# Kernel optimization log

Measured on AMD Instinct MI355X. Metric: run time of the kernel, lower is better.

The kernel has to match this reference:

```python
import jax, jax.numpy as jnp
import numpy as np

B, T, C = 4, 2048, 768
H = 12
D = C // H  # head dim 64

def setup_inputs() -> dict:
    key = jax.random.key(0)
    ks = jax.random.split(key, 6)
    scale = 1.0 / np.sqrt(C)
    x = jax.random.normal(ks[0], (B, T, C), dtype=jnp.float32)
    attention_mask = jax.random.randint(ks[1], (B, T), 0, 2, dtype=jnp.int64)
    Wqkv = jax.random.normal(ks[2], (C, 3 * C), dtype=jnp.float32) * scale
    bqkv = jax.random.normal(ks[3], (3 * C,), dtype=jnp.float32) * 0.02
    Wo = jax.random.normal(ks[4], (C, C), dtype=jnp.float32) * scale
    bo = jax.random.normal(ks[5], (C,), dtype=jnp.float32) * 0.02
    return {"x": x, "attention_mask": attention_mask, "Wqkv": Wqkv,
            "bqkv": bqkv, "Wo": Wo, "bo": bo}

def reference(x, attention_mask, Wqkv, bqkv, Wo, bo):
    # fused QKV projection: [B,T,3C]
    qkv = jnp.einsum('btc,cd->btd', x, Wqkv) + bqkv
    q, k, v = jnp.split(qkv, 3, axis=-1)
    # reshape to [B,H,T,D]
    q = q.reshape(B, T, H, D).transpose(0, 2, 1, 3)
    k = k.reshape(B, T, H, D).transpose(0, 2, 1, 3)
    v = v.reshape(B, T, H, D).transpose(0, 2, 1, 3)
    # module quirk: True (attended) where attention_mask == 0
    keep = (attention_mask == 0)[:, None, None, :]  # [B,1,1,T]
    scores = jnp.einsum('bhqd,bhkd->bhqk', q, k) / np.sqrt(D)
    scores = jnp.where(keep, scores, jnp.finfo(scores.dtype).min)
    probs = jax.nn.softmax(scores, axis=-1)
    context = jnp.einsum('bhqk,bhkd->bhqd', probs, v)
    context = context.transpose(0, 2, 1, 3).reshape(B, T, C)
    return jnp.einsum('btc,cd->btd', context, Wo) + bo
```

## Files before the change

kernel.cpp:

```cpp
#include <hip/hip_runtime.h>
#include <stdint.h>

#define AS1 __attribute__((address_space(1)))
#define AS3 __attribute__((address_space(3)))

typedef _Float16 f16;
typedef _Float16 f16x8 __attribute__((ext_vector_type(8)));
typedef _Float16 f16x4 __attribute__((ext_vector_type(4)));
typedef _Float16 f16x2 __attribute__((ext_vector_type(2)));
typedef float    f32x4  __attribute__((ext_vector_type(4)));
typedef float    f32x16 __attribute__((ext_vector_type(16)));

#define B_  4
#define T_  2048
#define C_  768
#define H_  12
#define D_  64
#define M_  (B_*T_)
#define N1_ (3*C_)

__device__ __forceinline__ void g2l16(const void* g, void* l) {
  __builtin_amdgcn_global_load_lds((const AS1 void*)g, (AS3 void*)l, 16, 0, 0);
}

__device__ __forceinline__ f32x4 fzero4() { f32x4 z = {0.f, 0.f, 0.f, 0.f}; return z; }

__device__ __forceinline__ f16x2 pk_f16(float a, float b) {
  auto t = __builtin_amdgcn_cvt_pkrtz(a, b);
  return *(f16x2*)&t;
}

__global__ __launch_bounds__(256)
void transpose_cvt_k(const float* __restrict__ in, f16* __restrict__ out, int R, int C) {
  __shared__ float tile[32][33];
  const int tx = threadIdx.x & 31, ty = threadIdx.x >> 5;
  const int c0 = blockIdx.x * 32, r0 = blockIdx.y * 32;
#pragma unroll
  for (int i = 0; i < 32; i += 8)
    tile[ty + i][tx] = in[(long)(r0 + ty + i) * C + c0 + tx];
  __syncthreads();
#pragma unroll
  for (int i = 0; i < 32; i += 8)
    out[(long)(c0 + ty + i) * R + r0 + tx] = (f16)tile[tx][ty + i];
}

__global__ __launch_bounds__(256)
void convert_f32_f16(const float* __restrict__ in, f16* __restrict__ out) {
  const int i = (blockIdx.x * 256 + threadIdx.x) * 4;
  const float4 v = *(const float4*)(in + i);
  f16x4 o = {(f16)v.x, (f16)v.y, (f16)v.z, (f16)v.w};
  *(f16x4*)(out + i) = o;
}

__global__ __launch_bounds__(256)
void init_idx_kernel(int* __restrict__ idx, int* __restrict__ cnt) {
  const int g = blockIdx.x * 256 + threadIdx.x;
  idx[g] = 0;
  if (g < B_) cnt[g] = 0;
}

__global__ __launch_bounds__(256)
void compact_kernel(const int* __restrict__ mask, int* __restrict__ idx,
                    int* __restrict__ cnt) {
  const int b = blockIdx.y;
  const int t = blockIdx.x * 256 + threadIdx.x;
  if (mask[b * T_ + t] == 0) {
    const int s = atomicAdd(&cnt[b], 1);
    idx[b * T_ + s] = t;
  }
}

__global__ __launch_bounds__(256)
void build_vt_gather(const f16* __restrict__ qkv, const int* __restrict__ idx,
                     const int* __restrict__ cnt, f16* __restrict__ vt) {
  __shared__ f16 tile[32][33];
  const int z = blockIdx.z, b = z / H_, h = z % H_;
  const int s0 = blockIdx.x * 32, d0 = blockIdx.y * 32;
  if (s0 >= cnt[b]) return;
  const int tx = threadIdx.x & 31, ty = threadIdx.x >> 5;
  const int* idx_b = idx + b * T_;
  f16* dst = vt + (long)z * D_ * T_;
#pragma unroll
  for (int i = 0; i < 32; i += 8) {
    const int t = idx_b[s0 + ty + i];
    tile[ty + i][tx] = qkv[(long)(b * T_ + t) * N1_ + 2 * C_ + h * D_ + d0 + tx];
  }
  __syncthreads();
#pragma unroll
  for (int i = 0; i < 32; i += 8)
    dst[(long)(d0 + ty + i) * T_ + s0 + tx] = tile[tx][ty + i];
}

template <typename OutT>
__global__ __launch_bounds__(256)
void gemm_bias_kernel(const f16* __restrict__ A, const f16* __restrict__ Bt,
                      const float* __restrict__ bias, OutT* __restrict__ Cc,
                      int K, int ldc) {
  __shared__ f16 lA[128 * 32];
  __shared__ f16 lB[128 * 32];
  const int tid = threadIdx.x;
  const int n0 = blockIdx.x * 128, m0 = blockIdx.y * 128;
  const int lane = tid & 63, w = tid >> 6;
  const int wm = (w & 1) * 64, wn = (w >> 1) * 64;
  const int r15 = lane & 15, q4 = lane >> 4;

  const int c0 = tid, c1 = 256 + tid;
  const int ar0 = c0 >> 2, ak0 = (c0 & 3) * 8;
  const int ar1 = c1 >> 2, ak1 = (c1 & 3) * 8;
  const f16* Ab = A + (long)m0 * K;
  const f16* Bb = Bt + (long)n0 * K;

  f32x4 acc[4][4];
#pragma unroll
  for (int i = 0; i < 4; i++)
#pragma unroll
    for (int j = 0; j < 4; j++) acc[i][j] = fzero4();

  for (int kb = 0; kb < K; kb += 32) {
    g2l16(Ab + (long)ar0 * K + kb + ak0, &lA[c0 * 8]);
    g2l16(Ab + (long)ar1 * K + kb + ak1, &lA[c1 * 8]);
    g2l16(Bb + (long)ar0 * K + kb + ak0, &lB[c0 * 8]);
    g2l16(Bb + (long)ar1 * K + kb + ak1, &lB[c1 * 8]);
    __syncthreads();
    f16x8 af[4], bfv[4];
#pragma unroll
    for (int mi = 0; mi < 4; mi++)
      af[mi] = *(const f16x8*)&lA[(wm + mi * 16 + r15) * 32 + q4 * 8];
#pragma unroll
    for (int ni = 0; ni < 4; ni++)
      bfv[ni] = *(const f16x8*)&lB[(wn + ni * 16 + r15) * 32 + q4 * 8];
#pragma unroll
    for (int mi = 0; mi < 4; mi++)
#pragma unroll
      for (int ni = 0; ni < 4; ni++)
        acc[mi][ni] = __builtin_amdgcn_mfma_f32_16x16x32_f16(af[mi], bfv[ni], acc[mi][ni], 0, 0, 0);
    __syncthreads();
  }

#pragma unroll
  for (int ni = 0; ni < 4; ni++) {
    const int col = n0 + wn + ni * 16 + r15;
    const float bs = bias[col];
#pragma unroll
    for (int mi = 0; mi < 4; mi++) {
#pragma unroll
      for (int r = 0; r < 4; r++) {
        const int row = m0 + wm + mi * 16 + q4 * 4 + r;
        Cc[(long)row * ldc + col] = (OutT)(acc[mi][ni][r] + bs);
      }
    }
  }
}

__global__ __launch_bounds__(256, 4)
void attn_kernel(const f16* __restrict__ qkv, const f16* __restrict__ vtc,
                 const int* __restrict__ idx, const int* __restrict__ cnt,
                 f16* __restrict__ ctx) {
  const int LDS_ = 72;
  __shared__ f16 QPs[128 * 72];
  __shared__ f16 Ks[64 * 72], Vs[64 * 72];
  const int tid = threadIdx.x, lane = tid & 63, w = tid >> 6;
  const int l31 = lane & 31, hh = lane >> 5;
  const int bh = blockIdx.y, b = bh / H_, h = bh % H_;
  const int q0 = blockIdx.x * 128;
  const f16* Qg = qkv + (long)(b * T_ + q0) * N1_ + h * D_;
  const f16* Kbase = qkv + (long)b * T_ * N1_ + C_ + h * D_;
  const f16* Vg = vtc + (long)bh * D_ * T_;
  const int* idx_b = idx + b * T_;
  const int nk = cnt[b];
  const int nkt = (nk + 63) >> 6;

  const f16 qsc = (f16)0.18033688f;
#pragma unroll
  for (int i = 0; i < 4; i++) {
    int c = i * 256 + tid, r = c >> 3, dcq = (c & 7) * 8;
    f16x8 v = *(const f16x8*)(Qg + (long)r * N1_ + dcq);
#pragma unroll
    for (int j = 0; j < 8; j++) v[j] = v[j] * qsc;
    *(f16x8*)&QPs[r * LDS_ + dcq] = v;
  }
  __syncthreads();
  f16x8 bq[4];
#pragma unroll
  for (int j = 0; j < 4; j++)
    bq[j] = *(const f16x8*)&QPs[(w * 32 + l31) * LDS_ + j * 16 + hh * 8];

  const int r0 = tid >> 3, r1 = 32 + (tid >> 3), dc = (tid & 7) * 8;
  int idxp0 = idx_b[r0], idxp1 = idx_b[r1];

  float l_acc = 0.f;
  f32x16 O[2];
#pragma unroll
  for (int dt = 0; dt < 2; dt++)
#pragma unroll
    for (int r = 0; r < 16; r++) O[dt][r] = 0.f;

  for (int kt = 0; kt < (nkt << 6); kt += 64) {
    __syncthreads();
    {
      const int t0 = idxp0, t1 = idxp1;
      f16x8 kv0 = *(const f16x8*)(Kbase + (long)t0 * N1_ + dc);
      f16x8 kv1 = *(const f16x8*)(Kbase + (long)t1 * N1_ + dc);
      f16x8 vv0 = *(const f16x8*)(Vg + (long)r0 * T_ + kt + dc);
      f16x8 vv1 = *(const f16x8*)(Vg + (long)r1 * T_ + kt + dc);
      idxp0 = idx_b[min(kt + 64 + r0, T_ - 1)];
      idxp1 = idx_b[min(kt + 64 + r1, T_ - 1)];
      *(f16x8*)&Ks[r0 * LDS_ + dc] = kv0;
      *(f16x8*)&Ks[r1 * LDS_ + dc] = kv1;
      *(f16x8*)&Vs[r0 * LDS_ + dc] = vv0;
      *(f16x8*)&Vs[r1 * LDS_ + dc] = vv1;
    }
    __syncthreads();

    const bool full = (kt + 64 <= nk);
#pragma unroll
    for (int ktile = 0; ktile < 2; ktile++) {
      f32x16 acc;
      if (full) {
#pragma unroll
        for (int r = 0; r < 16; r++) acc[r] = 0.f;
      } else {
        const int kbase = kt + ktile * 32 + hh * 4;
#pragma unroll
        for (int g = 0; g < 4; g++)
#pragma unroll
          for (int i = 0; i < 4; i++)
            acc[4 * g + i] = (kbase + 8 * g + i < nk) ? 0.f : -1e30f;
      }
#pragma unroll
      for (int j = 0; j < 4; j++) {
        f16x8 ak = *(const f16x8*)&Ks[(ktile * 32 + l31) * LDS_ + j * 16 + hh * 8];
        acc = __builtin_amdgcn_mfma_f32_32x32x16_f16(ak, bq[j], acc, 0, 0, 0);
      }
#pragma unroll
      for (int g = 0; g < 4; g++) {
        const float p0 = __builtin_amdgcn_exp2f(acc[4 * g + 0]);
        const float p1 = __builtin_amdgcn_exp2f(acc[4 * g + 1]);
        const float p2 = __builtin_amdgcn_exp2f(acc[4 * g + 2]);
        const float p3 = __builtin_amdgcn_exp2f(acc[4 * g + 3]);
        l_acc += (p0 + p1) + (p2 + p3);
        const f16x2 lo = pk_f16(p0, p1), hi = pk_f16(p2, p3);
        f16x4 pv; pv[0] = lo[0]; pv[1] = lo[1]; pv[2] = hi[0]; pv[3] = hi[1];
        *(f16x4*)&QPs[(w * 32 + l31) * LDS_ + ktile * 32 + g * 8 + hh * 4] = pv;
      }
    }
    asm volatile("s_waitcnt lgkmcnt(0)" ::: "memory");

#pragma unroll
    for (int j = 0; j < 4; j++) {
      f16x8 pa = *(const f16x8*)&QPs[(w * 32 + l31) * LDS_ + j * 16 + hh * 8];
#pragma unroll
      for (int dt = 0; dt < 2; dt++) {
        f16x8 vb = *(const f16x8*)&Vs[(dt * 32 + l31) * LDS_ + j * 16 + hh * 8];
        O[dt] = __builtin_amdgcn_mfma_f32_32x32x16_f16(pa, vb, O[dt], 0, 0, 0);
      }
    }
  }

  l_acc += __shfl_xor(l_acc, 32);
  float* Lw = (float*)&QPs[(w * 32) * LDS_];
  asm volatile("s_waitcnt lgkmcnt(0)" ::: "memory");
  if (hh == 0) Lw[l31] = l_acc;
  asm volatile("s_waitcnt lgkmcnt(0)" ::: "memory");
#pragma unroll
  for (int g = 0; g < 4; g++) {
    const f32x4 lv = *(const f32x4*)&Lw[g * 8 + hh * 4];
#pragma unroll
    for (int i = 0; i < 4; i++) {
      const float inv = 1.f / lv[i];
      const int row = b * T_ + q0 + w * 32 + g * 8 + hh * 4 + i;
#pragma unroll
      for (int dt = 0; dt < 2; dt++)
        ctx[(long)row * C_ + h * D_ + dt * 32 + l31] = (f16)(O[dt][4 * g + i] * inv);
    }
  }
}

extern "C" void kernel_launch(void* const* d_in, const int* in_sizes, int n_in,
                              void* d_out, int out_size, void* d_ws, size_t ws_size,
                              hipStream_t stream) {
  (void)in_sizes; (void)n_in; (void)out_size; (void)ws_size;
  const float* x    = (const float*)d_in[0];
  const int*   mask = (const int*)  d_in[1];
  const float* Wqkv = (const float*)d_in[2];
  const float* bqkv = (const float*)d_in[3];
  const float* Wo   = (const float*)d_in[4];
  const float* bo   = (const float*)d_in[5];
  float* out = (float*)d_out;

  char* ws = (char*)d_ws;
  const size_t OFF_WQKVT = 0;
  const size_t OFF_WOT   = OFF_WQKVT + 3538944;
  const size_t OFF_QKV   = OFF_WOT + 1179648;
  const size_t OFF_VT    = OFF_QKV + 37748736;
  const size_t OFF_XH    = OFF_VT + 12582912;
  const size_t OFF_IDX   = OFF_XH + 12582912;
  const size_t OFF_CNT   = OFF_IDX + 32768;
  f16* WqkvT = (f16*)(ws + OFF_WQKVT);
  f16* WoT   = (f16*)(ws + OFF_WOT);
  f16* qkv   = (f16*)(ws + OFF_QKV);
  f16* Vtc   = (f16*)(ws + OFF_VT);
  f16* xh    = (f16*)(ws + OFF_XH);
  f16* ctx   = (f16*)(ws + OFF_XH);
  int* idx   = (int*)(ws + OFF_IDX);
  int* cnt   = (int*)(ws + OFF_CNT);

  transpose_cvt_k<<<dim3(72, 24), 256, 0, stream>>>(Wqkv, WqkvT, 768, 2304);
  transpose_cvt_k<<<dim3(24, 24), 256, 0, stream>>>(Wo, WoT, 768, 768);
  convert_f32_f16<<<dim3(M_ * C_ / 1024), 256, 0, stream>>>(x, xh);
  init_idx_kernel<<<dim3(B_ * T_ / 256), 256, 0, stream>>>(idx, cnt);
  compact_kernel<<<dim3(T_ / 256, B_), 256, 0, stream>>>(mask, idx, cnt);
  gemm_bias_kernel<f16><<<dim3(18, 64), 256, 0, stream>>>(xh, WqkvT, bqkv, qkv, 768, 2304);
  build_vt_gather<<<dim3(64, 2, 48), 256, 0, stream>>>(qkv, idx, cnt, Vtc);
  attn_kernel<<<dim3(16, 48), 256, 0, stream>>>(qkv, Vtc, idx, cnt, ctx);
  gemm_bias_kernel<float><<<dim3(6, 64), 256, 0, stream>>>(ctx, WoT, bo, out, 768, 768);
}
```

Before: 215.0 us.

## Compute K/V projection only for kept tokens and store compacted K/V

The QKV GEMM is split so Q is computed for all rows, while K and V are computed only for unmasked tokens, using the compacted index list as a row gather on A. K and V are then written in compacted, contiguous form, so the attention kernel no longer does indexed gathers for K and build_vt reads V sequentially. This skips roughly half of the K/V projection work and makes K loads in attention contiguous. It relies on padding tiles (rows past cnt) being consistent, since the tail of the last tile reads padded idx entries that are set to zero.

```diff
diff --git a/kernel.cpp b/kernel.cpp
--- a/kernel.cpp
+++ b/kernel.cpp
@@ -71,20 +71,17 @@
 }
 
 __global__ __launch_bounds__(256)
-void build_vt_gather(const f16* __restrict__ qkv, const int* __restrict__ idx,
-                     const int* __restrict__ cnt, f16* __restrict__ vt) {
+void build_vt(const f16* __restrict__ Vc, const int* __restrict__ cnt,
+              f16* __restrict__ vt) {
   __shared__ f16 tile[32][33];
   const int z = blockIdx.z, b = z / H_, h = z % H_;
   const int s0 = blockIdx.x * 32, d0 = blockIdx.y * 32;
-  if (s0 >= cnt[b]) return;
+  if (s0 >= ((cnt[b] + 63) & ~63)) return;
   const int tx = threadIdx.x & 31, ty = threadIdx.x >> 5;
-  const int* idx_b = idx + b * T_;
   f16* dst = vt + (long)z * D_ * T_;
 #pragma unroll
-  for (int i = 0; i < 32; i += 8) {
-    const int t = idx_b[s0 + ty + i];
-    tile[ty + i][tx] = qkv[(long)(b * T_ + t) * N1_ + 2 * C_ + h * D_ + d0 + tx];
-  }
+  for (int i = 0; i < 32; i += 8)
+    tile[ty + i][tx] = Vc[(long)(b * T_ + s0 + ty + i) * C_ + h * D_ + d0 + tx];
   __syncthreads();
 #pragma unroll
   for (int i = 0; i < 32; i += 8)
@@ -152,9 +149,95 @@
   }
 }
 
+__global__ __launch_bounds__(256)
+void gemm_qkv_kernel(const f16* __restrict__ A, const f16* __restrict__ Bt,
+                     const float* __restrict__ bias, f16* __restrict__ Qb,
+                     f16* __restrict__ Kc, f16* __restrict__ Vc,
+                     const int* __restrict__ idx, const int* __restrict__ cnt) {
+  const int K = C_;
+  __shared__ f16 lA[128 * 32];
+  __shared__ f16 lB[128 * 32];
+  const int tid = threadIdx.x;
+  const bool isQ = blockIdx.x < 6;
+  const int n0 = (isQ ? blockIdx.x : blockIdx.x - 6) * 128;
+  const int lane = tid & 63, w = tid >> 6;
+  const int wm = (w & 1) * 64, wn = (w >> 1) * 64;
+  const int r15 = lane & 15, q4 = lane >> 4;
+
+  const int c0 = tid, c1 = 256 + tid;
+  const int ar0 = c0 >> 2, ak0 = (c0 & 3) * 8;
+  const int ar1 = c1 >> 2, ak1 = (c1 & 3) * 8;
+
+  int b = 0, s0 = 0;
+  long grow0, grow1;
+  if (isQ) {
+    const int m0 = blockIdx.y * 128;
+    grow0 = m0 + ar0;
+    grow1 = m0 + ar1;
+  } else {
+    b = blockIdx.y >> 4;
+    s0 = (blockIdx.y & 15) * 128;
+    if (s0 >= cnt[b]) return;
+    const int* idx_b = idx + b * T_;
+    grow0 = b * T_ + idx_b[s0 + ar0];
+    grow1 = b * T_ + idx_b[s0 + ar1];
+  }
+  const f16* A0 = A + grow0 * K;
+  const f16* A1 = A + grow1 * K;
+  const f16* Bb = Bt + (long)((isQ ? 0 : C_) + n0) * K;
+
+  f32x4 acc[4][4];
+#pragma unroll
+  for (int i = 0; i < 4; i++)
+#pragma unroll
+    for (int j = 0; j < 4; j++) acc[i][j] = fzero4();
+
+  for (int kb = 0; kb < K; kb += 32) {
+    g2l16(A0 + kb + ak0, &lA[c0 * 8]);
+    g2l16(A1 + kb + ak1, &lA[c1 * 8]);
+    g2l16(Bb + (long)ar0 * K + kb + ak0, &lB[c0 * 8]);
+    g2l16(Bb + (long)ar1 * K + kb + ak1, &lB[c1 * 8]);
+    __syncthreads();
+    f16x8 af[4], bfv[4];
+#pragma unroll
+    for (int mi = 0; mi < 4; mi++)
+      af[mi] = *(const f16x8*)&lA[(wm + mi * 16 + r15) * 32 + q4 * 8];
+#pragma unroll
+    for (int ni = 0; ni < 4; ni++)
+      bfv[ni] = *(const f16x8*)&lB[(wn + ni * 16 + r15) * 32 + q4 * 8];
+#pragma unroll
+    for (int mi = 0; mi < 4; mi++)
+#pragma unroll
+      for (int ni = 0; ni < 4; ni++)
+        acc[mi][ni] = __builtin_amdgcn_mfma_f32_16x16x32_f16(af[mi], bfv[ni], acc[mi][ni], 0, 0, 0);
+    __syncthreads();
+  }
+
+#pragma unroll
+  for (int ni = 0; ni < 4; ni++) {
+    const int col = n0 + wn + ni * 16 + r15;
+    const float bs = bias[isQ ? col : C_ + col];
+    f16* outp;
+    int ocol;
+    if (isQ)            { outp = Qb; ocol = col; }
+    else if (col < C_)  { outp = Kc; ocol = col; }
+    else                { outp = Vc; ocol = col - C_; }
+#pragma unroll
+    for (int mi = 0; mi < 4; mi++) {
+#pragma unroll
+      for (int r = 0; r < 4; r++) {
+        const int lrow = wm + mi * 16 + q4 * 4 + r;
+        const long row = isQ ? (long)blockIdx.y * 128 + lrow
+                             : (long)b * T_ + s0 + lrow;
+        outp[row * C_ + ocol] = (f16)(acc[mi][ni][r] + bs);
+      }
+    }
+  }
+}
+
 __global__ __launch_bounds__(256, 4)
-void attn_kernel(const f16* __restrict__ qkv, const f16* __restrict__ vtc,
-                 const int* __restrict__ idx, const int* __restrict__ cnt,
+void attn_kernel(const f16* __restrict__ Qb, const f16* __restrict__ Kc,
+                 const f16* __restrict__ vtc, const int* __restrict__ cnt,
                  f16* __restrict__ ctx) {
   const int LDS_ = 72;
   __shared__ f16 QPs[128 * 72];
@@ -163,10 +246,9 @@
   const int l31 = lane & 31, hh = lane >> 5;
   const int bh = blockIdx.y, b = bh / H_, h = bh % H_;
   const int q0 = blockIdx.x * 128;
-  const f16* Qg = qkv + (long)(b * T_ + q0) * N1_ + h * D_;
-  const f16* Kbase = qkv + (long)b * T_ * N1_ + C_ + h * D_;
+  const f16* Qg = Qb + (long)(b * T_ + q0) * C_ + h * D_;
+  const f16* Kbase = Kc + (long)b * T_ * C_ + h * D_;
   const f16* Vg = vtc + (long)bh * D_ * T_;
-  const int* idx_b = idx + b * T_;
   const int nk = cnt[b];
   const int nkt = (nk + 63) >> 6;
 
@@ -174,7 +256,7 @@
 #pragma unroll
   for (int i = 0; i < 4; i++) {
     int c = i * 256 + tid, r = c >> 3, dcq = (c & 7) * 8;
-    f16x8 v = *(const f16x8*)(Qg + (long)r * N1_ + dcq);
+    f16x8 v = *(const f16x8*)(Qg + (long)r * C_ + dcq);
 #pragma unroll
     for (int j = 0; j < 8; j++) v[j] = v[j] * qsc;
     *(f16x8*)&QPs[r * LDS_ + dcq] = v;
@@ -186,7 +268,6 @@
     bq[j] = *(const f16x8*)&QPs[(w * 32 + l31) * LDS_ + j * 16 + hh * 8];
 
   const int r0 = tid >> 3, r1 = 32 + (tid >> 3), dc = (tid & 7) * 8;
-  int idxp0 = idx_b[r0], idxp1 = idx_b[r1];
 
   float l_acc = 0.f;
   f32x16 O[2];
@@ -198,13 +279,10 @@
   for (int kt = 0; kt < (nkt << 6); kt += 64) {
     __syncthreads();
     {
-      const int t0 = idxp0, t1 = idxp1;
-      f16x8 kv0 = *(const f16x8*)(Kbase + (long)t0 * N1_ + dc);
-      f16x8 kv1 = *(const f16x8*)(Kbase + (long)t1 * N1_ + dc);
+      f16x8 kv0 = *(const f16x8*)(Kbase + (long)(kt + r0) * C_ + dc);
+      f16x8 kv1 = *(const f16x8*)(Kbase + (long)(kt + r1) * C_ + dc);
       f16x8 vv0 = *(const f16x8*)(Vg + (long)r0 * T_ + kt + dc);
       f16x8 vv1 = *(const f16x8*)(Vg + (long)r1 * T_ + kt + dc);
-      idxp0 = idx_b[min(kt + 64 + r0, T_ - 1)];
-      idxp1 = idx_b[min(kt + 64 + r1, T_ - 1)];
       *(f16x8*)&Ks[r0 * LDS_ + dc] = kv0;
       *(f16x8*)&Ks[r1 * LDS_ + dc] = kv1;
       *(f16x8*)&Vs[r0 * LDS_ + dc] = vv0;
@@ -291,14 +369,18 @@
   char* ws = (char*)d_ws;
   const size_t OFF_WQKVT = 0;
   const size_t OFF_WOT   = OFF_WQKVT + 3538944;
-  const size_t OFF_QKV   = OFF_WOT + 1179648;
-  const size_t OFF_VT    = OFF_QKV + 37748736;
+  const size_t OFF_Q     = OFF_WOT + 1179648;
+  const size_t OFF_KC    = OFF_Q + 12582912;
+  const size_t OFF_VC    = OFF_KC + 12582912;
+  const size_t OFF_VT    = OFF_VC + 12582912;
   const size_t OFF_XH    = OFF_VT + 12582912;
   const size_t OFF_IDX   = OFF_XH + 12582912;
   const size_t OFF_CNT   = OFF_IDX + 32768;
   f16* WqkvT = (f16*)(ws + OFF_WQKVT);
   f16* WoT   = (f16*)(ws + OFF_WOT);
-  f16* qkv   = (f16*)(ws + OFF_QKV);
+  f16* Qb    = (f16*)(ws + OFF_Q);
+  f16* Kc    = (f16*)(ws + OFF_KC);
+  f16* Vc    = (f16*)(ws + OFF_VC);
   f16* Vtc   = (f16*)(ws + OFF_VT);
   f16* xh    = (f16*)(ws + OFF_XH);
   f16* ctx   = (f16*)(ws + OFF_XH);
@@ -310,8 +392,8 @@
   convert_f32_f16<<<dim3(M_ * C_ / 1024), 256, 0, stream>>>(x, xh);
   init_idx_kernel<<<dim3(B_ * T_ / 256), 256, 0, stream>>>(idx, cnt);
   compact_kernel<<<dim3(T_ / 256, B_), 256, 0, stream>>>(mask, idx, cnt);
-  gemm_bias_kernel<f16><<<dim3(18, 64), 256, 0, stream>>>(xh, WqkvT, bqkv, qkv, 768, 2304);
-  build_vt_gather<<<dim3(64, 2, 48), 256, 0, stream>>>(qkv, idx, cnt, Vtc);
-  attn_kernel<<<dim3(16, 48), 256, 0, stream>>>(qkv, Vtc, idx, cnt, ctx);
+  gemm_qkv_kernel<<<dim3(18, 64), 256, 0, stream>>>(xh, WqkvT, bqkv, Qb, Kc, Vc, idx, cnt);
+  build_vt<<<dim3(64, 2, 48), 256, 0, stream>>>(Vc, cnt, Vtc);
+  attn_kernel<<<dim3(16, 48), 256, 0, stream>>>(Qb, Kc, Vtc, cnt, ctx);
   gemm_bias_kernel<float><<<dim3(6, 64), 256, 0, stream>>>(ctx, WoT, bo, out, 768, 768);
 }
```

Result: faster. 206.5 us (-4.0%).
